# Kernel optimization log

Measured on AMD Instinct MI355X. Metric: run time of the kernel, lower is better.

The kernel has to match this reference:

```python
import jax, jax.numpy as jnp
import numpy as np

B, H, C, Q = 32, 128, 2048, 256
NEG = -1e30


def setup_inputs() -> dict:
    key = jax.random.key(0)
    ks = jax.random.split(key, 8)
    context = jax.random.normal(ks[0], (B, H, C), dtype=jnp.float32)
    question = jax.random.normal(ks[1], (B, H, Q), dtype=jnp.float32)
    context_word_mask = jax.random.randint(ks[2], (B, C), 0, 2).astype(jnp.int32)
    question_word_mask = jax.random.randint(ks[3], (B, Q), 0, 2).astype(jnp.int32)
    # trilinear similarity params (QANet): S = c.w_c + q.w_q + (c*q).w_cq + bias
    scale = 1.0 / np.sqrt(H)
    w_c = jax.random.normal(ks[4], (H,), dtype=jnp.float32) * scale
    w_q = jax.random.normal(ks[5], (H,), dtype=jnp.float32) * scale
    w_cq = jax.random.normal(ks[6], (H,), dtype=jnp.float32) * scale
    bias = jnp.zeros((), dtype=jnp.float32)
    return {"context": context, "question": question,
            "context_word_mask": context_word_mask,
            "question_word_mask": question_word_mask,
            "w_c": w_c, "w_q": w_q, "w_cq": w_cq, "bias": bias}


def reference(context, question, context_word_mask, question_word_mask, w_c, w_q, w_cq, bias):
    # context: [B,H,C], question: [B,H,Q]
    # Trilinear similarity S[b,i,j] without materializing tiled [B,C,Q,H] tensors:
    part_c = jnp.einsum('bhi,h->bi', context, w_c)            # [B,C]
    part_q = jnp.einsum('bhj,h->bj', question, w_q)           # [B,Q]
    part_cq = jnp.einsum('bhi,bhj->bij', context * w_cq[None, :, None], question)  # [B,C,Q]
    S = part_cq + part_c[:, :, None] + part_q[:, None, :] + bias  # [B,C,Q]

    q_mask = question_word_mask[:, None, :].astype(bool)      # [B,1,Q]
    c_mask = context_word_mask[:, :, None].astype(bool)       # [B,C,1]
    S_row_norm = jax.nn.softmax(jnp.where(q_mask, S, NEG), axis=2)      # softmax over Q
    S_col_norm_T = jnp.swapaxes(jax.nn.softmax(jnp.where(c_mask, S, NEG), axis=1), 1, 2)  # [B,Q,C]

    context_t = jnp.swapaxes(context, 1, 2)    # [B,C,H]
    question_t = jnp.swapaxes(question, 1, 2)  # [B,Q,H]

    c2q = jnp.swapaxes(jnp.einsum('bij,bjh->bih', S_row_norm, question_t), 1, 2)  # [B,H,C]
    q2c = jnp.swapaxes(
        jnp.einsum('bik,bkh->bih', jnp.einsum('bij,bjk->bik', S_row_norm, S_col_norm_T), context_t),
        1, 2)  # [B,H,C]
    return (context, c2q, context * c2q, context * q2c)
```

## Files before the change

kernel.cpp:

```cpp
#include <hip/hip_runtime.h>
#include <hip/hip_bf16.h>
#include <math.h>


constexpr int kB = 32, kH = 128, kC = 2048, kQ = 256;
constexpr int kColChunks = 128;
constexpr float kNEG = -1e30f;

typedef short bf16x8 __attribute__((ext_vector_type(8)));
typedef float f32x4 __attribute__((ext_vector_type(4)));

static __device__ __forceinline__ unsigned short f2bf(float f) {
    __hip_bfloat16 h = __float2bfloat16(f);
    return __builtin_bit_cast(unsigned short, h);
}
static __device__ __forceinline__ float bf2f(unsigned short u) {
    unsigned int x = ((unsigned int)u) << 16;
    return __builtin_bit_cast(float, x);
}

__global__ __launch_bounds__(256) void k_prep_q(const float* __restrict__ q,
                                                const float* __restrict__ w_q,
                                                unsigned short* __restrict__ qT,
                                                unsigned short* __restrict__ qB,
                                                float* __restrict__ part_q) {
    int j0 = blockIdx.x * 64, b = blockIdx.y;
    __shared__ unsigned short tile[64 * 136];
    __shared__ float pcp[4][64];
    int t = threadIdx.x;
    int jl = t & 63, hg = t >> 6, hb = hg * 2;
    float accq = 0.f;
#pragma unroll
    for (int r = 0; r < 16; ++r) {
        int h = r * 8 + hb;
        float v0 = q[((size_t)b * kH + h) * kQ + j0 + jl];
        float v1 = q[((size_t)b * kH + h + 1) * kQ + j0 + jl];
        accq += v0 * w_q[h] + v1 * w_q[h + 1];
        qB[((size_t)b * kH + h) * kQ + j0 + jl]     = f2bf(v0);
        qB[((size_t)b * kH + h + 1) * kQ + j0 + jl] = f2bf(v1);
        unsigned int pk = (unsigned int)f2bf(v0) | ((unsigned int)f2bf(v1) << 16);
        *(unsigned int*)&tile[jl * 136 + h] = pk;
    }
    pcp[hg][jl] = accq;
    __syncthreads();
    if (t < 64) part_q[b * kQ + j0 + t] = pcp[0][t] + pcp[1][t] + pcp[2][t] + pcp[3][t];
#pragma unroll
    for (int r = 0; r < 4; ++r) {
        int idx = r * 256 + t;
        int j = idx >> 4, hc = (idx & 15) * 8;
        *(bf16x8*)&qT[((size_t)b * kQ + j0 + j) * kH + hc] =
            *(const bf16x8*)&tile[j * 136 + hc];
    }
}

__global__ __launch_bounds__(256) void k_Ssoft(const float* __restrict__ ctx,
                                               const unsigned short* __restrict__ qT,
                                               const float* __restrict__ w_c,
                                               const float* __restrict__ w_cq,
                                               const float* __restrict__ part_q,
                                               const float* __restrict__ bias,
                                               const int* __restrict__ qmask,
                                               const int* __restrict__ cmask,
                                               unsigned short* __restrict__ Eb,
                                               float* __restrict__ rowinv,
                                               float* __restrict__ ps) {
    int i0 = blockIdx.x * 64, b = blockIdx.y;
    __shared__ unsigned short Bs[256 * 40];
    __shared__ float smpq[256];
    __shared__ int smqm[256];
    __shared__ float smwc[128];
    __shared__ float smwq[128];
    __shared__ float smpc[64];
    int t = threadIdx.x;
    int lane = t & 63, w = t >> 6;
    int lrow = lane & 15, q4 = lane >> 4, kgrp = q4 * 8;
    smpq[t] = part_q[b * kQ + t];
    smqm[t] = qmask[b * kQ + t];
    if (t < 128) smwc[t] = w_c[t];
    else smwq[t - 128] = w_cq[t - 128];
    __syncthreads();

    const float* cbase = ctx + (size_t)b * kH * kC + i0 + w * 16 + lrow;
    float pcl = 0.f;

    f32x4 acc[16];
#pragma unroll
    for (int nt = 0; nt < 16; ++nt) acc[nt] = (f32x4){0.f, 0.f, 0.f, 0.f};

#pragma unroll
    for (int kk = 0; kk < 4; ++kk) {
        int h0 = kk * 32;
        bf16x8 af;
#pragma unroll
        for (int e = 0; e < 8; ++e) {
            int h = h0 + kgrp + e;
            float v = cbase[(size_t)h * kC];
            pcl += v * smwc[h];
            af[e] = (short)f2bf(v * smwq[h]);
        }
#pragma unroll
        for (int r2 = 0; r2 < 4; ++r2) {
            int idx = r2 * 256 + t;
            int jB = idx >> 2, hcB = (idx & 3) * 8;
            *(bf16x8*)&Bs[jB * 40 + hcB] =
                *(const bf16x8*)&qT[((size_t)b * kQ + jB) * kH + h0 + hcB];
        }
        __syncthreads();
#pragma unroll
        for (int nt = 0; nt < 16; ++nt) {
            bf16x8 bf = *(const bf16x8*)&Bs[(nt * 16 + lrow) * 40 + kgrp];
            acc[nt] = __builtin_amdgcn_mfma_f32_16x16x32_bf16(af, bf, acc[nt], 0, 0, 0);
        }
        __syncthreads();
    }

    pcl += __shfl_xor(pcl, 16);
    pcl += __shfl_xor(pcl, 32);
    if (q4 == 0) smpc[w * 16 + lrow] = pcl;
    __syncthreads();

    float bs = bias[0];
    float pq[16];
    int qm[16];
#pragma unroll
    for (int nt = 0; nt < 16; ++nt) {
        int col = nt * 16 + lrow;
        pq[nt] = smpq[col];
        qm[nt] = smqm[col];
    }
    int rowbase = i0 + w * 16 + q4 * 4;
    float pc[4];
    int cmr[4];
#pragma unroll
    for (int r = 0; r < 4; ++r) {
        pc[r] = smpc[w * 16 + q4 * 4 + r] + bs;
        cmr[r] = cmask[b * kC + rowbase + r];
    }
#pragma unroll
    for (int nt = 0; nt < 16; ++nt)
#pragma unroll
        for (int r = 0; r < 4; ++r)
            acc[nt][r] += pc[r] + pq[nt];

    float cs[16];
#pragma unroll
    for (int nt = 0; nt < 16; ++nt) cs[nt] = 0.f;

#pragma unroll
    for (int r = 0; r < 4; ++r) {
        float rmax = kNEG;
#pragma unroll
        for (int nt = 0; nt < 16; ++nt)
            if (qm[nt]) rmax = fmaxf(rmax, acc[nt][r]);
        rmax = fmaxf(rmax, __shfl_xor(rmax, 1));
        rmax = fmaxf(rmax, __shfl_xor(rmax, 2));
        rmax = fmaxf(rmax, __shfl_xor(rmax, 4));
        rmax = fmaxf(rmax, __shfl_xor(rmax, 8));
        float e[16];
        float rsum = 0.f;
#pragma unroll
        for (int nt = 0; nt < 16; ++nt) {
            e[nt] = qm[nt] ? __expf(acc[nt][r] - rmax) : 0.f;
            rsum += e[nt];
        }
        rsum += __shfl_xor(rsum, 1);
        rsum += __shfl_xor(rsum, 2);
        rsum += __shfl_xor(rsum, 4);
        rsum += __shfl_xor(rsum, 8);
        float emax = __expf(rmax);
        float Z = rsum * emax;
        unsigned short* dst = Eb + ((size_t)b * kC + rowbase + r) * kQ;
#pragma unroll
        for (int nt = 0; nt < 16; ++nt)
            dst[nt * 16 + lrow] = f2bf(e[nt] * emax);
        if (lrow == 0)
            rowinv[b * kC + rowbase + r] = Z > 0.f ? 1.f / Z : 0.f;
        if (cmr[r]) {
#pragma unroll
            for (int nt = 0; nt < 16; ++nt)
                cs[nt] += e[nt] * emax;
        }
    }
#pragma unroll
    for (int nt = 0; nt < 16; ++nt) {
        cs[nt] += __shfl_xor(cs[nt], 16);
        cs[nt] += __shfl_xor(cs[nt], 32);
    }
    int chunk = blockIdx.x * 4 + w;
#pragma unroll
    for (int k = 0; k < 4; ++k) {
        int nt = q4 * 4 + k;
        int col = nt * 16 + lrow;
        ps[((size_t)b * kColChunks + chunk) * kQ + col] = cs[nt];
    }
}

__global__ __launch_bounds__(256) void k_colZ(const float* __restrict__ ps,
                                              float* __restrict__ colinv) {
    int id = blockIdx.x * 256 + threadIdx.x;
    int b = id / kQ, j = id % kQ;
    float s = 0.f;
#pragma unroll 8
    for (int c = 0; c < kColChunks; ++c)
        s += ps[((size_t)b * kColChunks + c) * kQ + j];
    colinv[id] = s > 0.f ? 1.f / s : 0.f;
}

__global__ __launch_bounds__(512) void k_T2_mfma(const unsigned short* __restrict__ Eb,
                                                 const float* __restrict__ ctx,
                                                 const int* __restrict__ cmask,
                                                 unsigned short* __restrict__ Tpart) {
    int chunk = blockIdx.x, b = blockIdx.y;
    __shared__ unsigned short Et[256 * 42];
    __shared__ unsigned short Bs[128 * 40];
    __shared__ int smc[256];
    int t = threadIdx.x;
    if (t < 256) smc[t] = cmask[b * kC + chunk * 256 + t];
    int lane = t & 63, wave = t >> 6;
    int wm = wave >> 1, wn = wave & 1;
    int lrow = lane & 15, kgrp = (lane >> 4) * 8;
    int ip = t >> 5, js2 = t & 31;
    int hB = t >> 2, isegB = (t & 3) * 8;

    f32x4 acc[2][8];
#pragma unroll
    for (int mt = 0; mt < 2; ++mt)
#pragma unroll
        for (int nt = 0; nt < 8; ++nt)
            acc[mt][nt] = (f32x4){0.f, 0.f, 0.f, 0.f};
    __syncthreads();

    for (int kk = 0; kk < 8; ++kk) {
        int i0 = chunk * 256 + kk * 32;
        int li = kk * 32 + 2 * ip;
        unsigned int m0 = smc[li]     ? 0xFFFFFFFFu : 0u;
        unsigned int m1 = smc[li + 1] ? 0xFFFFFFFFu : 0u;
        const unsigned short* r0 = Eb + ((size_t)b * kC + i0 + 2 * ip) * kQ;
#pragma unroll
        for (int m = 0; m < 4; ++m) {
            int j = 2 * js2 + 64 * m;
            unsigned int a  = *(const unsigned int*)&r0[j] & m0;
            unsigned int bv = *(const unsigned int*)&r0[kQ + j] & m1;
            unsigned int lo = (a & 0xFFFFu) | (bv << 16);
            unsigned int hi = (a >> 16) | (bv & 0xFFFF0000u);
            *(unsigned int*)&Et[(size_t)j * 42 + 2 * ip]       = lo;
            *(unsigned int*)&Et[(size_t)(j + 1) * 42 + 2 * ip] = hi;
        }
        {
            const float* cb = ctx + ((size_t)b * kH + hB) * kC + i0 + isegB;
            float4 a0 = *(const float4*)cb;
            float4 a1 = *(const float4*)(cb + 4);
            float vv[8] = {a0.x, a0.y, a0.z, a0.w, a1.x, a1.y, a1.z, a1.w};
            bf16x8 p0;
#pragma unroll
            for (int e = 0; e < 8; ++e) p0[e] = (short)f2bf(vv[e]);
            *(bf16x8*)&Bs[hB * 40 + isegB] = p0;
        }
        __syncthreads();
        bf16x8 af[2], bfr[8];
#pragma unroll
        for (int mt = 0; mt < 2; ++mt)
            af[mt] = *(const bf16x8*)&Bs[(wm * 32 + mt * 16 + lrow) * 40 + kgrp];
#pragma unroll
        for (int nt = 0; nt < 8; ++nt)
            bfr[nt] = *(const bf16x8*)&Et[(size_t)(wn * 128 + nt * 16 + lrow) * 42 + kgrp];
#pragma unroll
        for (int nt = 0; nt < 8; ++nt)
#pragma unroll
            for (int mt = 0; mt < 2; ++mt)
                acc[mt][nt] = __builtin_amdgcn_mfma_f32_16x16x32_bf16(af[mt], bfr[nt], acc[mt][nt], 0, 0, 0);
        __syncthreads();
    }

    const size_t M = (size_t)kB * kH * kQ;
#pragma unroll
    for (int mt = 0; mt < 2; ++mt)
#pragma unroll
        for (int r = 0; r < 4; ++r) {
            int h = wm * 32 + mt * 16 + (lane >> 4) * 4 + r;
            unsigned short* dst = Tpart + (size_t)chunk * M + ((size_t)b * kH + h) * kQ + wn * 128 + lrow;
#pragma unroll
            for (int nt = 0; nt < 8; ++nt)
                dst[nt * 16] = f2bf(acc[mt][nt][r]);
        }
}

__global__ __launch_bounds__(256) void k_Tred(const unsigned short* __restrict__ Tpart,
                                              const float* __restrict__ colinv,
                                              unsigned short* __restrict__ Tb) {
    size_t id = (size_t)blockIdx.x * 256 + threadIdx.x;
    const size_t M = (size_t)kB * kH * kQ;
    int j = (int)(id % kQ);
    int b = (int)(id / ((size_t)kH * kQ));
    float s = 0.f;
#pragma unroll
    for (int c = 0; c < 8; ++c) s += bf2f(Tpart[c * M + id]);
    Tb[id] = f2bf(s * colinv[b * kQ + j]);
}

__global__ __launch_bounds__(256) void k_out_mfma(const unsigned short* __restrict__ Eb,
                                                  const unsigned short* __restrict__ qB,
                                                  const unsigned short* __restrict__ Tb,
                                                  const float* __restrict__ ctx,
                                                  const float* __restrict__ rowinv,
                                                  float* __restrict__ out) {
    int i0 = blockIdx.x * 64;
    int b  = blockIdx.y;
    __shared__ unsigned short As[64 * 40];
    __shared__ float stgC[64 * 68];
    __shared__ float stgT[64 * 68];
    int t = threadIdx.x;
    int rA = t >> 2, cA = (t & 3) * 8;
    int lane = t & 63, wave = t >> 6;
    int hw = wave * 32;
    int kgrp = (lane >> 4) * 8;
    int lrow = lane & 15, q4 = lane >> 4;

    f32x4 accC[4][2];
    f32x4 accT[4][2];
#pragma unroll
    for (int mt = 0; mt < 4; ++mt)
#pragma unroll
        for (int nt = 0; nt < 2; ++nt) {
            accC[mt][nt] = (f32x4){0.f, 0.f, 0.f, 0.f};
            accT[mt][nt] = (f32x4){0.f, 0.f, 0.f, 0.f};
        }

    for (int kk = 0; kk < 8; ++kk) {
        int j0 = kk * 32;
        *(bf16x8*)&As[rA * 40 + cA] =
            *(const bf16x8*)&Eb[((size_t)b * kC + i0 + rA) * kQ + j0 + cA];
        __syncthreads();
        bf16x8 af[4];
#pragma unroll
        for (int mt = 0; mt < 4; ++mt)
            af[mt] = *(const bf16x8*)&As[(mt * 16 + lrow) * 40 + kgrp];
#pragma unroll
        for (int nt = 0; nt < 2; ++nt) {
            int h = hw + nt * 16 + lrow;
            bf16x8 bq = *(const bf16x8*)&qB[((size_t)b * kH + h) * kQ + j0 + kgrp];
            bf16x8 bt = *(const bf16x8*)&Tb[((size_t)b * kH + h) * kQ + j0 + kgrp];
#pragma unroll
            for (int mt = 0; mt < 4; ++mt) {
                accC[mt][nt] = __builtin_amdgcn_mfma_f32_16x16x32_bf16(af[mt], bq, accC[mt][nt], 0, 0, 0);
                accT[mt][nt] = __builtin_amdgcn_mfma_f32_16x16x32_bf16(af[mt], bt, accT[mt][nt], 0, 0, 0);
            }
        }
        __syncthreads();
    }

    const size_t N = (size_t)kB * kH * kC;
    int ii = t & 63, hb = t >> 6;
    float riv = rowinv[b * kC + i0 + ii];
#pragma unroll
    for (int g = 0; g < 2; ++g) {
        if ((wave >> 1) == g) {
            int hloc = (wave & 1) * 32;
#pragma unroll
            for (int mt = 0; mt < 4; ++mt)
#pragma unroll
                for (int nt = 0; nt < 2; ++nt)
#pragma unroll
                    for (int r = 0; r < 4; ++r) {
                        int rowh = hloc + nt * 16 + lrow;
                        int coli = mt * 16 + q4 * 4 + r;
                        stgC[rowh * 68 + coli] = accC[mt][nt][r];
                        stgT[rowh * 68 + coli] = accT[mt][nt][r];
                    }
        }
        __syncthreads();
#pragma unroll 4
        for (int p = 0; p < 16; ++p) {
            int hl = hb + p * 4;
            int h = g * 64 + hl;
            float vc = stgC[hl * 68 + ii] * riv;
            float vt = stgT[hl * 68 + ii] * riv;
            size_t base = ((size_t)b * kH + h) * kC + i0 + ii;
            float c = ctx[base];
            out[base]         = c;
            out[N + base]     = vc;
            out[2 * N + base] = c * vc;
            out[3 * N + base] = c * vt;
        }
        __syncthreads();
    }
}

extern "C" void kernel_launch(void* const* d_in, const int* in_sizes, int n_in,
                              void* d_out, int out_size, void* d_ws, size_t ws_size,
                              hipStream_t stream) {
    const float* ctx   = (const float*)d_in[0];
    const float* q     = (const float*)d_in[1];
    const int*   cmask = (const int*)d_in[2];
    const int*   qmask = (const int*)d_in[3];
    const float* w_c   = (const float*)d_in[4];
    const float* w_q   = (const float*)d_in[5];
    const float* w_cq  = (const float*)d_in[6];
    const float* bias  = (const float*)d_in[7];
    float* out = (float*)d_out;

    unsigned short* Eb = (unsigned short*)d_ws;
    unsigned short* qB = Eb + (size_t)kB * kC * kQ;
    unsigned short* Tb = qB + (size_t)kB * kH * kQ;
    float* part_q = (float*)(Tb + (size_t)kB * kH * kQ);
    float* rowinv = part_q + kB * kQ;
    float* colinv = rowinv + kB * kC;
    float* ps     = colinv + kB * kQ;
    size_t need = (size_t)((char*)(ps + (size_t)kB * kColChunks * kQ) - (char*)d_ws);
    if (ws_size < need) return;

    const size_t N = (size_t)kB * kH * kC;
    unsigned short* Tpart = (unsigned short*)out;
    unsigned short* qT    = (unsigned short*)(out + 2 * N);

    k_prep_q<<<dim3(kQ / 64, kB), 256, 0, stream>>>(q, w_q, qT, qB, part_q);
    k_Ssoft<<<dim3(kC / 64, kB), 256, 0, stream>>>(ctx, qT, w_c, w_cq, part_q, bias,
                                                   qmask, cmask, Eb, rowinv, ps);
    k_colZ<<<kB * kQ / 256, 256, 0, stream>>>(ps, colinv);
    k_T2_mfma<<<dim3(8, kB), 512, 0, stream>>>(Eb, ctx, cmask, Tpart);
    k_Tred<<<kB * kH * kQ / 256, 256, 0, stream>>>(Tpart, colinv, Tb);
    k_out_mfma<<<dim3(kC / 64, kB), 256, 0, stream>>>(Eb, qB, Tb, ctx, rowinv, out);
}
```

Measured before the change: 112.2 us.

## Double-buffer question tiles, prefetch B fragments, and vectorize T reduction

In the similarity kernel the question-tile staging moves to a two-slot shared buffer, so the next slice is loaded while MFMAs consume the current one, and one barrier per iteration is dropped. The output kernel register-prefetches the next qB/Tb fragments one iteration ahead. The partial-T reduction kernel now handles four bf16 elements per thread with 64-bit loads and stores and launches a quarter as many blocks. The cost is more shared memory and registers, which may reduce occupancy.

```diff
diff --git a/kernel.cpp b/kernel.cpp
--- a/kernel.cpp
+++ b/kernel.cpp
@@ -65,7 +65,7 @@
                                                float* __restrict__ rowinv,
                                                float* __restrict__ ps) {
     int i0 = blockIdx.x * 64, b = blockIdx.y;
-    __shared__ unsigned short Bs[256 * 40];
+    __shared__ unsigned short Bs[2][256 * 40];
     __shared__ float smpq[256];
     __shared__ int smqm[256];
     __shared__ float smwc[128];
@@ -78,6 +78,14 @@
     smqm[t] = qmask[b * kQ + t];
     if (t < 128) smwc[t] = w_c[t];
     else smwq[t - 128] = w_cq[t - 128];
+
+    int jB = t >> 2, hcB = (t & 3) * 8;
+#pragma unroll
+    for (int r2 = 0; r2 < 4; ++r2) {
+        int jj = (r2 * 256 + t) >> 2, hh = ((r2 * 256 + t) & 3) * 8;
+        *(bf16x8*)&Bs[0][jj * 40 + hh] =
+            *(const bf16x8*)&qT[((size_t)b * kQ + jj) * kH + hh];
+    }
     __syncthreads();
 
     const float* cbase = ctx + (size_t)b * kH * kC + i0 + w * 16 + lrow;
@@ -90,6 +98,7 @@
 #pragma unroll
     for (int kk = 0; kk < 4; ++kk) {
         int h0 = kk * 32;
+        int cur = kk & 1;
         bf16x8 af;
 #pragma unroll
         for (int e = 0; e < 8; ++e) {
@@ -98,17 +107,18 @@
             pcl += v * smwc[h];
             af[e] = (short)f2bf(v * smwq[h]);
         }
-#pragma unroll
-        for (int r2 = 0; r2 < 4; ++r2) {
-            int idx = r2 * 256 + t;
-            int jB = idx >> 2, hcB = (idx & 3) * 8;
-            *(bf16x8*)&Bs[jB * 40 + hcB] =
-                *(const bf16x8*)&qT[((size_t)b * kQ + jB) * kH + h0 + hcB];
-        }
-        __syncthreads();
+        if (kk < 3) {
+            int h1 = h0 + 32;
+#pragma unroll
+            for (int r2 = 0; r2 < 4; ++r2) {
+                int jj = (r2 * 256 + t) >> 2, hh = ((r2 * 256 + t) & 3) * 8;
+                *(bf16x8*)&Bs[cur ^ 1][jj * 40 + hh] =
+                    *(const bf16x8*)&qT[((size_t)b * kQ + jj) * kH + h1 + hh];
+            }
+        }
 #pragma unroll
         for (int nt = 0; nt < 16; ++nt) {
-            bf16x8 bf = *(const bf16x8*)&Bs[(nt * 16 + lrow) * 40 + kgrp];
+            bf16x8 bf = *(const bf16x8*)&Bs[cur][(nt * 16 + lrow) * 40 + kgrp];
             acc[nt] = __builtin_amdgcn_mfma_f32_16x16x32_bf16(af, bf, acc[nt], 0, 0, 0);
         }
         __syncthreads();
@@ -288,14 +298,24 @@
 __global__ __launch_bounds__(256) void k_Tred(const unsigned short* __restrict__ Tpart,
                                               const float* __restrict__ colinv,
                                               unsigned short* __restrict__ Tb) {
-    size_t id = (size_t)blockIdx.x * 256 + threadIdx.x;
+    size_t id4 = ((size_t)blockIdx.x * 256 + threadIdx.x) * 4;
     const size_t M = (size_t)kB * kH * kQ;
-    int j = (int)(id % kQ);
-    int b = (int)(id / ((size_t)kH * kQ));
-    float s = 0.f;
-#pragma unroll
-    for (int c = 0; c < 8; ++c) s += bf2f(Tpart[c * M + id]);
-    Tb[id] = f2bf(s * colinv[b * kQ + j]);
+    int j = (int)(id4 & (kQ - 1));
+    int b = (int)(id4 / ((size_t)kH * kQ));
+    float s0 = 0.f, s1 = 0.f, s2 = 0.f, s3 = 0.f;
+#pragma unroll
+    for (int c = 0; c < 8; ++c) {
+        uint2 v = *(const uint2*)&Tpart[c * M + id4];
+        s0 += bf2f((unsigned short)(v.x & 0xFFFFu));
+        s1 += bf2f((unsigned short)(v.x >> 16));
+        s2 += bf2f((unsigned short)(v.y & 0xFFFFu));
+        s3 += bf2f((unsigned short)(v.y >> 16));
+    }
+    const float* ci = colinv + b * kQ + j;
+    uint2 o;
+    o.x = (unsigned int)f2bf(s0 * ci[0]) | ((unsigned int)f2bf(s1 * ci[1]) << 16);
+    o.y = (unsigned int)f2bf(s2 * ci[2]) | ((unsigned int)f2bf(s3 * ci[3]) << 16);
+    *(uint2*)&Tb[id4] = o;
 }
 
 __global__ __launch_bounds__(256) void k_out_mfma(const unsigned short* __restrict__ Eb,
@@ -326,8 +346,27 @@
             accT[mt][nt] = (f32x4){0.f, 0.f, 0.f, 0.f};
         }
 
+    bf16x8 bqn[2], btn[2];
+#pragma unroll
+    for (int nt = 0; nt < 2; ++nt) {
+        int h = hw + nt * 16 + lrow;
+        bqn[nt] = *(const bf16x8*)&qB[((size_t)b * kH + h) * kQ + kgrp];
+        btn[nt] = *(const bf16x8*)&Tb[((size_t)b * kH + h) * kQ + kgrp];
+    }
+
     for (int kk = 0; kk < 8; ++kk) {
         int j0 = kk * 32;
+        bf16x8 bqc[2] = {bqn[0], bqn[1]};
+        bf16x8 btc[2] = {btn[0], btn[1]};
+        if (kk < 7) {
+            int j1 = j0 + 32;
+#pragma unroll
+            for (int nt = 0; nt < 2; ++nt) {
+                int h = hw + nt * 16 + lrow;
+                bqn[nt] = *(const bf16x8*)&qB[((size_t)b * kH + h) * kQ + j1 + kgrp];
+                btn[nt] = *(const bf16x8*)&Tb[((size_t)b * kH + h) * kQ + j1 + kgrp];
+            }
+        }
         *(bf16x8*)&As[rA * 40 + cA] =
             *(const bf16x8*)&Eb[((size_t)b * kC + i0 + rA) * kQ + j0 + cA];
         __syncthreads();
@@ -337,13 +376,10 @@
             af[mt] = *(const bf16x8*)&As[(mt * 16 + lrow) * 40 + kgrp];
 #pragma unroll
         for (int nt = 0; nt < 2; ++nt) {
-            int h = hw + nt * 16 + lrow;
-            bf16x8 bq = *(const bf16x8*)&qB[((size_t)b * kH + h) * kQ + j0 + kgrp];
-            bf16x8 bt = *(const bf16x8*)&Tb[((size_t)b * kH + h) * kQ + j0 + kgrp];
 #pragma unroll
             for (int mt = 0; mt < 4; ++mt) {
-                accC[mt][nt] = __builtin_amdgcn_mfma_f32_16x16x32_bf16(af[mt], bq, accC[mt][nt], 0, 0, 0);
-                accT[mt][nt] = __builtin_amdgcn_mfma_f32_16x16x32_bf16(af[mt], bt, accT[mt][nt], 0, 0, 0);
+                accC[mt][nt] = __builtin_amdgcn_mfma_f32_16x16x32_bf16(af[mt], bqc[nt], accC[mt][nt], 0, 0, 0);
+                accT[mt][nt] = __builtin_amdgcn_mfma_f32_16x16x32_bf16(af[mt], btc[nt], accT[mt][nt], 0, 0, 0);
             }
         }
         __syncthreads();
@@ -418,6 +454,6 @@
                                                    qmask, cmask, Eb, rowinv, ps);
     k_colZ<<<kB * kQ / 256, 256, 0, stream>>>(ps, colinv);
     k_T2_mfma<<<dim3(8, kB), 512, 0, stream>>>(Eb, ctx, cmask, Tpart);
-    k_Tred<<<kB * kH * kQ / 256, 256, 0, stream>>>(Tpart, colinv, Tb);
+    k_Tred<<<kB * kH * kQ / 1024, 256, 0, stream>>>(Tpart, colinv, Tb);
     k_out_mfma<<<dim3(kC / 64, kB), 256, 0, stream>>>(Eb, qB, Tb, ctx, rowinv, out);
 }
```

Result: slower. 118.4 us (+5.5%).
